# Optimization experiments

Measured on AMD Instinct MI355X. Metric: run time of the kernel, lower is better.

## Reference

```python
import jax, jax.numpy as jnp
import numpy as np

TEMPERATURE = 0.07
MASK_VAL = -65504.0  # torch code's fill value (fp16 min), note: applied BEFORE temperature division
EPS = 1e-8


def setup_inputs() -> dict:
    key = jax.random.key(0)
    z = jax.random.normal(key, (8192, 1024), dtype=jnp.float32)
    return {"z": z}


def reference(z):
    N = z.shape[0]
    # cosine similarity via normalized GEMM (torch clamps norm at eps)
    norms = jnp.maximum(jnp.linalg.norm(z, axis=-1, keepdims=True), EPS)
    zn = z / norms
    cos_sim = zn @ zn.T  # [N, N]
    eye = jnp.eye(N, dtype=bool)
    cos_sim = jnp.where(eye, MASK_VAL, cos_sim) / TEMPERATURE
    # pos_mask = eye rolled by N//2 along dim 0 -> pos_mask[i, (i - N//2) % N] = True
    idx = jnp.arange(N)
    pos = cos_sim[idx, (idx - N // 2) % N]
    nll = -pos + jax.nn.logsumexp(cos_sim, axis=-1)
    return nll.mean()
```

## Files before the change

### kernel.cpp

```cpp
#include <hip/hip_runtime.h>
#include <hip/hip_bf16.h>


#define N 8192
#define D 1024
#define INV_T 14.285714285714286f
#define NTILES 2080
#define ACC_SCALE (INV_T / 1024.0f)

typedef float f32x4 __attribute__((ext_vector_type(4)));
typedef long lx2 __attribute__((ext_vector_type(2)));

__device__ inline void gload16(const void* g, void* l) {
  __builtin_amdgcn_global_load_lds(
      (const __attribute__((address_space(1))) void*)g,
      (__attribute__((address_space(3))) void*)l, 16, 0, 0);
}

__global__ __launch_bounds__(256) void k_normalize(const float* __restrict__ z,
                                                   unsigned char* __restrict__ zn8,
                                                   float* __restrict__ rowsum) {
  const int gt = blockIdx.x * 256 + threadIdx.x;
  if (gt < N) rowsum[gt] = 0.0f;
  const int row = gt >> 6;
  const int l = threadIdx.x & 63;
  const float4* zr = (const float4*)(z + (size_t)row * D);
  float4 v[4];
  float ss = 0.f;
#pragma unroll
  for (int j = 0; j < 4; ++j) {
    v[j] = zr[l + 64 * j];
    ss += v[j].x * v[j].x + v[j].y * v[j].y + v[j].z * v[j].z + v[j].w * v[j].w;
  }
#pragma unroll
  for (int off = 32; off > 0; off >>= 1) ss += __shfl_xor(ss, off, 64);
  const float sc = 32.0f / fmaxf(sqrtf(ss), 1e-8f);
  int* orow = (int*)(zn8 + (size_t)row * D);
#pragma unroll
  for (int j = 0; j < 4; ++j) {
    int p = __builtin_amdgcn_cvt_pk_fp8_f32(v[j].x * sc, v[j].y * sc, 0, false);
    p = __builtin_amdgcn_cvt_pk_fp8_f32(v[j].z * sc, v[j].w * sc, p, true);
    orow[l + 64 * j] = p;
  }
}

__global__ __launch_bounds__(512, 4) void k_tile(const unsigned char* __restrict__ zn8,
                                                 float* __restrict__ rowsum,
                                                 float* __restrict__ pos) {
  extern __shared__ __align__(16) char smem[];
  const int tid = threadIdx.x;
  const int w = tid >> 6, l = tid & 63;

  const int b = blockIdx.x;
  int tr = (int)((sqrtf(8.0f * (float)b + 1.0f) - 1.0f) * 0.5f);
  if (tr * (tr + 1) / 2 > b) --tr;
  if ((tr + 1) * (tr + 2) / 2 <= b) ++tr;
  const int tc = b - tr * (tr + 1) / 2;
  const bool diag = (tr == tc);

  const int wr = w >> 1, wc = w & 1;
  const int m = l & 15, kg = l >> 4;
  const int rowA0 = tr * 128, colB0 = tc * 128;

  f32x4 acc[2][4] = {};

  int srow[2], scol[2];
#pragma unroll
  for (int j = 0; j < 2; ++j) {
    int s = j * 512 + tid;
    int r = s >> 3;
    srow[j] = r;
    scol[j] = (s & 7) ^ (r & 7);
  }

  const int csw0 = (kg ^ (m & 7)) * 16;
  const int csw1 = ((kg + 4) ^ (m & 7)) * 16;

  {
    char* ab = smem;
    char* bb = smem + 16384;
#pragma unroll
    for (int j = 0; j < 2; ++j) {
      const int s = j * 512 + tid;
      gload16((const char*)zn8 + ((size_t)(rowA0 + srow[j]) * D + scol[j] * 16), ab + s * 16);
    }
    if (!diag) {
#pragma unroll
      for (int j = 0; j < 2; ++j) {
        const int s = j * 512 + tid;
        gload16((const char*)zn8 + ((size_t)(colB0 + srow[j]) * D + scol[j] * 16), bb + s * 16);
      }
    }
  }
  __syncthreads();

  for (int kt = 0; kt < 8; ++kt) {
    if (kt < 7) {
      const size_t kb = (size_t)(kt + 1) * 128;
      char* ab = smem + ((kt + 1) & 1) * 32768;
#pragma unroll
      for (int j = 0; j < 2; ++j) {
        const int s = j * 512 + tid;
        gload16((const char*)zn8 + ((size_t)(rowA0 + srow[j]) * D + kb + scol[j] * 16), ab + s * 16);
      }
      if (!diag) {
        char* bb = ab + 16384;
#pragma unroll
        for (int j = 0; j < 2; ++j) {
          const int s = j * 512 + tid;
          gload16((const char*)zn8 + ((size_t)(colB0 + srow[j]) * D + kb + scol[j] * 16), bb + s * 16);
        }
      }
    }
    const char* ab = smem + (kt & 1) * 32768;
    const char* bb = diag ? ab : (ab + 16384);

    lx2 a0[2], a1[2];
#pragma unroll
    for (int mt = 0; mt < 2; ++mt) {
      const char* rp = ab + (wr * 32 + mt * 16 + m) * 128;
      a0[mt] = *(const lx2*)(rp + csw0);
      a1[mt] = *(const lx2*)(rp + csw1);
    }
#pragma unroll
    for (int nt = 0; nt < 4; ++nt) {
      const char* rp = bb + (wc * 64 + nt * 16 + m) * 128;
      const lx2 b0 = *(const lx2*)(rp + csw0);
      const lx2 b1 = *(const lx2*)(rp + csw1);
#pragma unroll
      for (int mt = 0; mt < 2; ++mt) {
        acc[mt][nt] = __builtin_amdgcn_mfma_f32_16x16x32_fp8_fp8(a0[mt].x, b0.x, acc[mt][nt], 0, 0, 0);
        acc[mt][nt] = __builtin_amdgcn_mfma_f32_16x16x32_fp8_fp8(a0[mt].y, b0.y, acc[mt][nt], 0, 0, 0);
        acc[mt][nt] = __builtin_amdgcn_mfma_f32_16x16x32_fp8_fp8(a1[mt].x, b1.x, acc[mt][nt], 0, 0, 0);
        acc[mt][nt] = __builtin_amdgcn_mfma_f32_16x16x32_fp8_fp8(a1[mt].y, b1.y, acc[mt][nt], 0, 0, 0);
      }
    }
    __syncthreads();
  }

  const int quad = l >> 4;
  const int col = l & 15;
  float cs[4] = {0.f, 0.f, 0.f, 0.f};
#pragma unroll
  for (int mt = 0; mt < 2; ++mt) {
    float rs[4] = {0.f, 0.f, 0.f, 0.f};
#pragma unroll
    for (int nt = 0; nt < 4; ++nt) {
      const int gcol = colB0 + wc * 64 + nt * 16 + col;
#pragma unroll
      for (int r = 0; r < 4; ++r) {
        const int grow = rowA0 + wr * 32 + mt * 16 + quad * 4 + r;
        const float t = acc[mt][nt][r] * ACC_SCALE;
        if (gcol == (grow ^ (N / 2))) {
          pos[grow] = t;
          pos[gcol] = t;
        }
        const float e = (gcol == grow) ? 0.0f : __expf(t - INV_T);
        rs[r] += e;
        cs[nt] += e;
      }
    }
#pragma unroll
    for (int off = 1; off < 16; off <<= 1) {
#pragma unroll
      for (int r = 0; r < 4; ++r) rs[r] += __shfl_xor(rs[r], off, 64);
    }
    if (col == 0) {
#pragma unroll
      for (int r = 0; r < 4; ++r)
        atomicAdd(&rowsum[rowA0 + wr * 32 + mt * 16 + quad * 4 + r], rs[r]);
    }
  }
  if (!diag) {
#pragma unroll
    for (int nt = 0; nt < 4; ++nt) {
      cs[nt] += __shfl_xor(cs[nt], 16, 64);
      cs[nt] += __shfl_xor(cs[nt], 32, 64);
    }
    if (l < 16) {
#pragma unroll
      for (int nt = 0; nt < 4; ++nt)
        atomicAdd(&rowsum[colB0 + wc * 64 + nt * 16 + l], cs[nt]);
    }
  }
}

__global__ __launch_bounds__(1024) void k_final(const float* __restrict__ rowsum,
                                                const float* __restrict__ pos,
                                                float* __restrict__ out) {
  const int t = threadIdx.x;
  float s = 0.f;
  for (int i = t; i < N; i += 1024) s += INV_T + __logf(rowsum[i]) - pos[i];
#pragma unroll
  for (int off = 32; off > 0; off >>= 1) s += __shfl_down(s, off, 64);
  __shared__ float red[16];
  if ((t & 63) == 0) red[t >> 6] = s;
  __syncthreads();
  if (t == 0) {
    float tot = 0.f;
#pragma unroll
    for (int j = 0; j < 16; ++j) tot += red[j];
    out[0] = tot * (1.0f / N);
  }
}

extern "C" void kernel_launch(void* const* d_in, const int* in_sizes, int n_in,
                              void* d_out, int out_size, void* d_ws, size_t ws_size,
                              hipStream_t stream) {
  const float* z = (const float*)d_in[0];
  float* out = (float*)d_out;
  char* ws = (char*)d_ws;
  unsigned char* zn8 = (unsigned char*)ws;
  float* rowsum = (float*)(ws + (size_t)N * D);
  float* pos = (float*)(ws + (size_t)N * D + (size_t)N * 4);

  static bool attr_set = false;
  if (!attr_set) {
    hipFuncSetAttribute((const void*)k_tile,
                        hipFuncAttributeMaxDynamicSharedMemorySize, 65536);
    attr_set = true;
  }

  k_normalize<<<N / 4, 256, 0, stream>>>(z, zn8, rowsum);
  k_tile<<<NTILES, 512, 65536, stream>>>(zn8, rowsum, pos);
  k_final<<<1, 1024, 0, stream>>>(rowsum, pos, out);
}
```

Measured before the change: 162.0 us.

## Use 256-row tiles with split off-diagonal work over symmetric GEMM

The symmetric upper-triangle tiling moves from 128x128 tiles (2080 blocks) to 256-row tiles. There are 32 diagonal 256x256 blocks, and each off-diagonal 256x256 tile is split into two 256x128 halves, for 1024 blocks in total. The larger tiles raise arithmetic intensity per byte loaded into LDS and cut the number of blocks and atomics. In exchange, each block uses more registers and 96KB of LDS, occupancy drops to 2 blocks per CU, and the diagonal blocks carry twice the work of the others, which risks load imbalance.

Result: faster. 157.8 us (-2.6%).

```diff
diff --git a/kernel.cpp b/kernel.cpp
--- a/kernel.cpp
+++ b/kernel.cpp
@@ -5,7 +5,7 @@
 #define N 8192
 #define D 1024
 #define INV_T 14.285714285714286f
-#define NTILES 2080
+#define NBLK 1024
 #define ACC_SCALE (INV_T / 1024.0f)
 
 typedef float f32x4 __attribute__((ext_vector_type(4)));
@@ -44,134 +44,203 @@
   }
 }
 
-__global__ __launch_bounds__(512, 4) void k_tile(const unsigned char* __restrict__ zn8,
+__global__ __launch_bounds__(512, 2) void k_tile(const unsigned char* __restrict__ zn8,
                                                  float* __restrict__ rowsum,
                                                  float* __restrict__ pos) {
   extern __shared__ __align__(16) char smem[];
   const int tid = threadIdx.x;
   const int w = tid >> 6, l = tid & 63;
-
-  const int b = blockIdx.x;
-  int tr = (int)((sqrtf(8.0f * (float)b + 1.0f) - 1.0f) * 0.5f);
-  if (tr * (tr + 1) / 2 > b) --tr;
-  if ((tr + 1) * (tr + 2) / 2 <= b) ++tr;
-  const int tc = b - tr * (tr + 1) / 2;
-  const bool diag = (tr == tc);
-
   const int wr = w >> 1, wc = w & 1;
   const int m = l & 15, kg = l >> 4;
-  const int rowA0 = tr * 128, colB0 = tc * 128;
-
-  f32x4 acc[2][4] = {};
-
-  int srow[2], scol[2];
-#pragma unroll
-  for (int j = 0; j < 2; ++j) {
+  const int quad = l >> 4, col = l & 15;
+
+  int srow[4], scol[4];
+#pragma unroll
+  for (int j = 0; j < 4; ++j) {
     int s = j * 512 + tid;
     int r = s >> 3;
     srow[j] = r;
     scol[j] = (s & 7) ^ (r & 7);
   }
-
   const int csw0 = (kg ^ (m & 7)) * 16;
   const int csw1 = ((kg + 4) ^ (m & 7)) * 16;
 
-  {
-    char* ab = smem;
-    char* bb = smem + 16384;
-#pragma unroll
-    for (int j = 0; j < 2; ++j) {
-      const int s = j * 512 + tid;
-      gload16((const char*)zn8 + ((size_t)(rowA0 + srow[j]) * D + scol[j] * 16), ab + s * 16);
-    }
-    if (!diag) {
+  const int b = blockIdx.x;
+
+  if (b < 32) {
+    const int rowA0 = b * 256, colB0 = b * 256;
+    f32x4 acc[4][8] = {};
+
+    {
+      char* ab = smem;
+#pragma unroll
+      for (int j = 0; j < 4; ++j) {
+        const int s = j * 512 + tid;
+        gload16((const char*)zn8 + ((size_t)(rowA0 + srow[j]) * D + scol[j] * 16), ab + s * 16);
+      }
+    }
+    __syncthreads();
+
+    for (int kt = 0; kt < 8; ++kt) {
+      if (kt < 7) {
+        const size_t kb = (size_t)(kt + 1) * 128;
+        char* ab = smem + ((kt + 1) & 1) * 49152;
+#pragma unroll
+        for (int j = 0; j < 4; ++j) {
+          const int s = j * 512 + tid;
+          gload16((const char*)zn8 + ((size_t)(rowA0 + srow[j]) * D + kb + scol[j] * 16), ab + s * 16);
+        }
+      }
+      const char* ab = smem + (kt & 1) * 49152;
+
+      lx2 a0[4], a1[4];
+#pragma unroll
+      for (int mt = 0; mt < 4; ++mt) {
+        const char* rp = ab + (wr * 64 + mt * 16 + m) * 128;
+        a0[mt] = *(const lx2*)(rp + csw0);
+        a1[mt] = *(const lx2*)(rp + csw1);
+      }
+#pragma unroll
+      for (int nt = 0; nt < 8; ++nt) {
+        const char* rp = ab + (wc * 128 + nt * 16 + m) * 128;
+        const lx2 b0 = *(const lx2*)(rp + csw0);
+        const lx2 b1 = *(const lx2*)(rp + csw1);
+#pragma unroll
+        for (int mt = 0; mt < 4; ++mt) {
+          acc[mt][nt] = __builtin_amdgcn_mfma_f32_16x16x32_fp8_fp8(a0[mt].x, b0.x, acc[mt][nt], 0, 0, 0);
+          acc[mt][nt] = __builtin_amdgcn_mfma_f32_16x16x32_fp8_fp8(a0[mt].y, b0.y, acc[mt][nt], 0, 0, 0);
+          acc[mt][nt] = __builtin_amdgcn_mfma_f32_16x16x32_fp8_fp8(a1[mt].x, b1.x, acc[mt][nt], 0, 0, 0);
+          acc[mt][nt] = __builtin_amdgcn_mfma_f32_16x16x32_fp8_fp8(a1[mt].y, b1.y, acc[mt][nt], 0, 0, 0);
+        }
+      }
+      __syncthreads();
+    }
+
+#pragma unroll
+    for (int mt = 0; mt < 4; ++mt) {
+      float rs[4] = {0.f, 0.f, 0.f, 0.f};
+#pragma unroll
+      for (int nt = 0; nt < 8; ++nt) {
+        const int gcol = colB0 + wc * 128 + nt * 16 + col;
+#pragma unroll
+        for (int r = 0; r < 4; ++r) {
+          const int grow = rowA0 + wr * 64 + mt * 16 + quad * 4 + r;
+          const float t = acc[mt][nt][r] * ACC_SCALE;
+          rs[r] += (gcol == grow) ? 0.0f : __expf(t - INV_T);
+        }
+      }
+#pragma unroll
+      for (int off = 1; off < 16; off <<= 1) {
+#pragma unroll
+        for (int r = 0; r < 4; ++r) rs[r] += __shfl_xor(rs[r], off, 64);
+      }
+      if (col == 0) {
+#pragma unroll
+        for (int r = 0; r < 4; ++r)
+          atomicAdd(&rowsum[rowA0 + wr * 64 + mt * 16 + quad * 4 + r], rs[r]);
+      }
+    }
+  } else {
+    int p = b - 32;
+    const int h = p & 1;
+    p >>= 1;
+    int tr = (int)((1.0f + sqrtf(8.0f * (float)p + 1.0f)) * 0.5f);
+    if (tr * (tr - 1) / 2 > p) --tr;
+    if (tr * (tr + 1) / 2 <= p) ++tr;
+    const int tc = p - tr * (tr - 1) / 2;
+    const int rowA0 = tr * 256, colB0 = tc * 256 + h * 128;
+
+    f32x4 acc[4][4] = {};
+
+    {
+      char* ab = smem;
+      char* bb = smem + 32768;
+#pragma unroll
+      for (int j = 0; j < 4; ++j) {
+        const int s = j * 512 + tid;
+        gload16((const char*)zn8 + ((size_t)(rowA0 + srow[j]) * D + scol[j] * 16), ab + s * 16);
+      }
 #pragma unroll
       for (int j = 0; j < 2; ++j) {
         const int s = j * 512 + tid;
         gload16((const char*)zn8 + ((size_t)(colB0 + srow[j]) * D + scol[j] * 16), bb + s * 16);
       }
     }
-  }
-  __syncthreads();
-
-  for (int kt = 0; kt < 8; ++kt) {
-    if (kt < 7) {
-      const size_t kb = (size_t)(kt + 1) * 128;
-      char* ab = smem + ((kt + 1) & 1) * 32768;
-#pragma unroll
-      for (int j = 0; j < 2; ++j) {
-        const int s = j * 512 + tid;
-        gload16((const char*)zn8 + ((size_t)(rowA0 + srow[j]) * D + kb + scol[j] * 16), ab + s * 16);
-      }
-      if (!diag) {
-        char* bb = ab + 16384;
+    __syncthreads();
+
+    for (int kt = 0; kt < 8; ++kt) {
+      if (kt < 7) {
+        const size_t kb = (size_t)(kt + 1) * 128;
+        char* ab = smem + ((kt + 1) & 1) * 49152;
+        char* bb = ab + 32768;
+#pragma unroll
+        for (int j = 0; j < 4; ++j) {
+          const int s = j * 512 + tid;
+          gload16((const char*)zn8 + ((size_t)(rowA0 + srow[j]) * D + kb + scol[j] * 16), ab + s * 16);
+        }
 #pragma unroll
         for (int j = 0; j < 2; ++j) {
           const int s = j * 512 + tid;
           gload16((const char*)zn8 + ((size_t)(colB0 + srow[j]) * D + kb + scol[j] * 16), bb + s * 16);
         }
       }
-    }
-    const char* ab = smem + (kt & 1) * 32768;
-    const char* bb = diag ? ab : (ab + 16384);
-
-    lx2 a0[2], a1[2];
-#pragma unroll
-    for (int mt = 0; mt < 2; ++mt) {
-      const char* rp = ab + (wr * 32 + mt * 16 + m) * 128;
-      a0[mt] = *(const lx2*)(rp + csw0);
-      a1[mt] = *(const lx2*)(rp + csw1);
-    }
-#pragma unroll
-    for (int nt = 0; nt < 4; ++nt) {
-      const char* rp = bb + (wc * 64 + nt * 16 + m) * 128;
-      const lx2 b0 = *(const lx2*)(rp + csw0);
-      const lx2 b1 = *(const lx2*)(rp + csw1);
-#pragma unroll
-      for (int mt = 0; mt < 2; ++mt) {
-        acc[mt][nt] = __builtin_amdgcn_mfma_f32_16x16x32_fp8_fp8(a0[mt].x, b0.x, acc[mt][nt], 0, 0, 0);
-        acc[mt][nt] = __builtin_amdgcn_mfma_f32_16x16x32_fp8_fp8(a0[mt].y, b0.y, acc[mt][nt], 0, 0, 0);
-        acc[mt][nt] = __builtin_amdgcn_mfma_f32_16x16x32_fp8_fp8(a1[mt].x, b1.x, acc[mt][nt], 0, 0, 0);
-        acc[mt][nt] = __builtin_amdgcn_mfma_f32_16x16x32_fp8_fp8(a1[mt].y, b1.y, acc[mt][nt], 0, 0, 0);
-      }
-    }
-    __syncthreads();
-  }
-
-  const int quad = l >> 4;
-  const int col = l & 15;
-  float cs[4] = {0.f, 0.f, 0.f, 0.f};
-#pragma unroll
-  for (int mt = 0; mt < 2; ++mt) {
-    float rs[4] = {0.f, 0.f, 0.f, 0.f};
-#pragma unroll
-    for (int nt = 0; nt < 4; ++nt) {
-      const int gcol = colB0 + wc * 64 + nt * 16 + col;
-#pragma unroll
-      for (int r = 0; r < 4; ++r) {
-        const int grow = rowA0 + wr * 32 + mt * 16 + quad * 4 + r;
-        const float t = acc[mt][nt][r] * ACC_SCALE;
-        if (gcol == (grow ^ (N / 2))) {
-          pos[grow] = t;
-          pos[gcol] = t;
-        }
-        const float e = (gcol == grow) ? 0.0f : __expf(t - INV_T);
-        rs[r] += e;
-        cs[nt] += e;
-      }
-    }
-#pragma unroll
-    for (int off = 1; off < 16; off <<= 1) {
-#pragma unroll
-      for (int r = 0; r < 4; ++r) rs[r] += __shfl_xor(rs[r], off, 64);
-    }
-    if (col == 0) {
-#pragma unroll
-      for (int r = 0; r < 4; ++r)
-        atomicAdd(&rowsum[rowA0 + wr * 32 + mt * 16 + quad * 4 + r], rs[r]);
-    }
-  }
-  if (!diag) {
+      const char* ab = smem + (kt & 1) * 49152;
+      const char* bb = ab + 32768;
+
+      lx2 a0[4], a1[4];
+#pragma unroll
+      for (int mt = 0; mt < 4; ++mt) {
+        const char* rp = ab + (wr * 64 + mt * 16 + m) * 128;
+        a0[mt] = *(const lx2*)(rp + csw0);
+        a1[mt] = *(const lx2*)(rp + csw1);
+      }
+#pragma unroll
+      for (int nt = 0; nt < 4; ++nt) {
+        const char* rp = bb + (wc * 64 + nt * 16 + m) * 128;
+        const lx2 b0 = *(const lx2*)(rp + csw0);
+        const lx2 b1 = *(const lx2*)(rp + csw1);
+#pragma unroll
+        for (int mt = 0; mt < 4; ++mt) {
+          acc[mt][nt] = __builtin_amdgcn_mfma_f32_16x16x32_fp8_fp8(a0[mt].x, b0.x, acc[mt][nt], 0, 0, 0);
+          acc[mt][nt] = __builtin_amdgcn_mfma_f32_16x16x32_fp8_fp8(a0[mt].y, b0.y, acc[mt][nt], 0, 0, 0);
+          acc[mt][nt] = __builtin_amdgcn_mfma_f32_16x16x32_fp8_fp8(a1[mt].x, b1.x, acc[mt][nt], 0, 0, 0);
+          acc[mt][nt] = __builtin_amdgcn_mfma_f32_16x16x32_fp8_fp8(a1[mt].y, b1.y, acc[mt][nt], 0, 0, 0);
+        }
+      }
+      __syncthreads();
+    }
+
+    float cs[4] = {0.f, 0.f, 0.f, 0.f};
+#pragma unroll
+    for (int mt = 0; mt < 4; ++mt) {
+      float rs[4] = {0.f, 0.f, 0.f, 0.f};
+#pragma unroll
+      for (int nt = 0; nt < 4; ++nt) {
+        const int gcol = colB0 + wc * 64 + nt * 16 + col;
+#pragma unroll
+        for (int r = 0; r < 4; ++r) {
+          const int grow = rowA0 + wr * 64 + mt * 16 + quad * 4 + r;
+          const float t = acc[mt][nt][r] * ACC_SCALE;
+          if (gcol == (grow ^ (N / 2))) {
+            pos[grow] = t;
+            pos[gcol] = t;
+          }
+          const float e = __expf(t - INV_T);
+          rs[r] += e;
+          cs[nt] += e;
+        }
+      }
+#pragma unroll
+      for (int off = 1; off < 16; off <<= 1) {
+#pragma unroll
+        for (int r = 0; r < 4; ++r) rs[r] += __shfl_xor(rs[r], off, 64);
+      }
+      if (col == 0) {
+#pragma unroll
+        for (int r = 0; r < 4; ++r)
+          atomicAdd(&rowsum[rowA0 + wr * 64 + mt * 16 + quad * 4 + r], rs[r]);
+      }
+    }
 #pragma unroll
     for (int nt = 0; nt < 4; ++nt) {
       cs[nt] += __shfl_xor(cs[nt], 16, 64);
@@ -217,11 +286,11 @@
   static bool attr_set = false;
   if (!attr_set) {
     hipFuncSetAttribute((const void*)k_tile,
-                        hipFuncAttributeMaxDynamicSharedMemorySize, 65536);
+                        hipFuncAttributeMaxDynamicSharedMemorySize, 98304);
     attr_set = true;
   }
 
   k_normalize<<<N / 4, 256, 0, stream>>>(z, zn8, rowsum);
-  k_tile<<<NTILES, 512, 65536, stream>>>(zn8, rowsum, pos);
+  k_tile<<<NBLK, 512, 98304, stream>>>(zn8, rowsum, pos);
   k_final<<<1, 1024, 0, stream>>>(rowsum, pos, out);
 }
```
